# Optimization experiments

Hardware: AMD Instinct MI355X
Metric: run time of the kernel (lower is better)

The kernel has to match this reference:

```python
import jax, jax.numpy as jnp
import numpy as np

PAD = 200000   # padding index = all_features_num
D = 128        # input_dim (embedding dim)
H = 256        # hidden_dim
K = 15         # item_num (top-k)
M = 4          # multi_head


def _cos(a, b, eps=1e-8):
    # torch.cosine_similarity semantics with eps clamp on norms
    na = jnp.maximum(jnp.linalg.norm(a, axis=-1), eps)
    nb = jnp.maximum(jnp.linalg.norm(b, axis=-1), eps)
    return jnp.sum(a * b, axis=-1) / (na * nb)


def _rnn_input(x, emb):
    # x: [..., T, F] int. Fields :-2 are embedded+summed, field -2 is time.
    t = x[..., -2].astype(jnp.float32)
    dt = jnp.concatenate([jnp.zeros_like(t[..., :1]), jnp.diff(t, axis=-1)], axis=-1)
    e = emb[x[..., :-2]].sum(axis=-2)          # [..., T, D]
    x_self = e[:, 0:1, -1:, :]                  # [B,1,1,D] (self item placed at last slot of session 0)
    return jnp.concatenate([e, dt[..., None]], axis=-1), x_self


def _time_rnn(seq, W, U, b, wt, return_all=False):
    # Time-aware GRU. seq: [N, T, in+1]; last channel is delta-time feeding a decay gate.
    f, dt = seq[..., :-1], seq[..., -1:]
    N = seq.shape[0]
    g_in = jnp.einsum('nti,ij->ntj', f, W) + b   # precompute input projections [N,T,3H]

    def step(h, inp):
        g, d = inp                               # g:[N,3H], d:[N,1]
        decay = jnp.exp(-jax.nn.relu(d * wt))    # time-aware decay of hidden state
        hd = h * decay
        u = hd @ U
        z = jax.nn.sigmoid(g[:, :H] + u[:, :H])
        r = jax.nn.sigmoid(g[:, H:2 * H] + u[:, H:2 * H])
        n = jnp.tanh(g[:, 2 * H:] + r * u[:, 2 * H:])
        h_new = (1.0 - z) * hd + z * n
        return h_new, h_new

    h0 = jnp.zeros((N, H), seq.dtype)
    h_last, hs = jax.lax.scan(step, h0, (jnp.swapaxes(g_in, 0, 1), jnp.swapaxes(dt, 0, 1)))
    return jnp.swapaxes(hs, 0, 1) if return_all else h_last


def setup_inputs() -> dict:
    key = jax.random.key(0)
    ks = jax.random.split(key, 20)
    def n(k, shape, s=0.05):
        return jax.random.normal(k, shape, jnp.float32) * s
    x = jax.random.randint(ks[0], (512, 16, 64, 8), 0, PAD, dtype=jnp.int32)
    x_continuous = jax.random.randint(ks[1], (128, 128, 8), 0, PAD, dtype=jnp.int32)
    self_loc = jax.random.randint(ks[2], (512,), 0, 64, dtype=jnp.int32)
    emb = n(ks[3], (PAD + 1, D)).at[PAD].set(0.0)  # padding_idx row = 0
    return {
        'x': x, 'x_continuous': x_continuous, 'self_loc': self_loc, 'emb': emb,
        'W_rnn': n(ks[4], (2 * D, 3 * H)), 'U_rnn': n(ks[5], (H, 3 * H)), 'b_rnn': n(ks[6], (3 * H,)),
        'wt_rnn': jax.random.uniform(ks[7], (H,), jnp.float32, 0.0, 1e-5),
        'W_c': n(ks[8], (D, 3 * H)), 'U_c': n(ks[9], (H, 3 * H)), 'b_c': n(ks[10], (3 * H,)),
        'wt_c': jax.random.uniform(ks[11], (H,), jnp.float32, 0.0, 1e-5),
        'Wv': n(ks[12], (2 * H, M)), 'bv': n(ks[13], (M,)),
        'W0': n(ks[14], (D + (2 + M) * H, 1024)), 'b0': n(ks[15], (1024,)),
        'W1': n(ks[16], (1024, 512)), 'b1': n(ks[17], (512,)),
        'W2': n(ks[18], (512, 256)), 'b2': n(ks[19], (256,)),
        'Wp': n(jax.random.fold_in(key, 99), (256, 1)), 'bp': jnp.zeros((1,), jnp.float32),
    }


def reference(x, x_continuous, self_loc, emb, W_rnn, U_rnn, b_rnn, wt_rnn,
              W_c, U_c, b_c, wt_c, Wv, bv, W0, b0, W1, b1, W2, b2, Wp, bp):
    B = x.shape[0]
    label_len = B // x_continuous.shape[0]
    # ---- get_top_k: cosine sim + topk + gather ----
    real = x[..., 0] != PAD                         # [B,S,L]
    bidx = jnp.arange(B)
    e_self = emb[x[bidx, 0, self_loc, -3]]           # [B,D]
    e_items = emb[x[..., -3]]                        # [B,S,L,D]
    cos = _cos(e_self[:, None, None, :], e_items)    # [B,S,L]
    neg = jnp.min(jnp.where(real, cos, jnp.inf)) - 1.0
    sim = jnp.where(real, cos, neg)
    top_idx = jnp.sort(jax.lax.top_k(sim, K)[1], axis=-1)      # [B,S,K]
    x_top = jnp.take_along_axis(x, top_idx[..., None], axis=2)  # [B,S,K,F]
    x_top = x_top.at[:, 0, -1].set(x[bidx, 0, self_loc])
    # ---- rnn inputs ----
    xs, x_self = _rnn_input(x_top, emb)              # [B,S,K,D+1], [B,1,1,D]
    xs = jnp.concatenate([jnp.broadcast_to(x_self, xs.shape[:-1] + (D,)), xs], axis=-1)
    xs = xs.reshape(-1, K, 2 * D + 1)                # [B*S,K,2D+1]
    xc, _ = _rnn_input(x_continuous[:, None], emb)
    xc = xc[:, 0]                                    # [B',L2,D+1]
    # ---- RNNs ----
    h = _time_rnn(xs, W_rnn, U_rnn, b_rnn, wt_rnn).reshape(B, -1, H)   # [B,S,H]
    h_cont = _time_rnn(xc, W_c, U_c, b_c, wt_c, return_all=True)[:, -label_len:, :].reshape(B, H)
    # ---- multi-head attention over sessions ----
    a1 = jnp.concatenate([h, jnp.broadcast_to(h[:, :1], h.shape)], axis=-1) @ Wv + bv  # [B,S,M]
    a2 = jax.nn.softmax(jnp.tanh(a1), axis=1)
    h_att = jnp.einsum('bsm,bsh->bmh', a2, h).reshape(B, M * H)
    hh = jnp.concatenate([x_self.reshape(B, D), h[:, 0], h_att, h_cont], axis=-1)
    # ---- predict MLP (dropout = identity in eval) ----
    lr = lambda v: jnp.where(v > 0, v, 0.01 * v)     # LeakyReLU(0.01)
    z = lr(hh @ W0 + b0)
    z = lr(z @ W1 + b1)
    z = lr(z @ W2 + b2)
    return jax.nn.sigmoid(z @ Wp + bp)               # [B,1]
```

## Files before the change

kernel.cpp:

```cpp
#include <hip/hip_runtime.h>
#include <hip/hip_bf16.h>


#define PAD_TOK 200000
#define DD 128
#define HH 256
#define KK 15
#define BB 512
#define SS 16
#define II 64

typedef __bf16 bf16x8 __attribute__((ext_vector_type(8)));
typedef __bf16 bf16x4 __attribute__((ext_vector_type(4)));
typedef float f32x4 __attribute__((ext_vector_type(4)));
#define MFMA16 __builtin_amdgcn_mfma_f32_16x16x32_bf16
#define MFMA8 __builtin_amdgcn_mfma_f32_16x16x32_fp8_fp8

__device__ __forceinline__ float sigm(float x) { return 1.f / (1.f + __expf(-x)); }
__device__ __forceinline__ float tanh_fast(float x) {
  x = fminf(fmaxf(x, -15.f), 15.f);
  float e2 = __expf(2.f * x);
  return (e2 - 1.f) / (e2 + 1.f);
}
__device__ __forceinline__ float bfu(unsigned u16) { return __uint_as_float(u16 << 16); }
// ... 94 lines not shown
  if (tid < 64) {
    unsigned m = smin[tid];
    for (int o = 32; o; o >>= 1) m = min(m, __shfl_xor(m, o));
    if (tid == 0 && m != 0xFFFFFFFFu) atomicMin(minu, m);
  }
}

__global__ __launch_bounds__(64) void k_topk(const int* __restrict__ x,
                                             const float* __restrict__ simw,
                                             const unsigned* __restrict__ minu,
                                             int* __restrict__ topidx) {
  int row = blockIdx.x, i = threadIdx.x;
  unsigned mk = *minu;
  float neg = ((mk & 0x80000000u) ? __uint_as_float(mk ^ 0x80000000u) : __uint_as_float(~mk)) - 1.0f;
  float c = simw[(size_t)row * II + i];
  bool real = x[((size_t)row * II + i) * 8] != PAD_TOK;
  float s = real ? c : neg;
  __shared__ float sv[64];
  sv[i] = s;
  __syncthreads();
  int rank = 0;
  for (int j = 0; j < 64; ++j) {
    float o = sv[j];
    rank += (o > s) || (o == s && j < i);
  }
  bool sel = rank < KK;
  unsigned long long mask = __ballot(sel);
  if (sel) {
    int pos = __popcll(mask & ((1ull << i) - 1ull));
    topidx[row * KK + pos] = i;
  }
}

__global__ __launch_bounds__(128) void k_xself(const int* __restrict__ x,
                                               const int* __restrict__ self_loc,
                                               const float* __restrict__ emb,
                                               float* __restrict__ xself,
                                               __bf16* __restrict__ xself_bf) {
  int b = blockIdx.x, d = threadIdx.x;
  const int* xr = x + ((size_t)(b * SS) * II + self_loc[b]) * 8;
  float acc = 0.f;
#pragma unroll
  for (int jj = 0; jj < 6; ++jj) acc += emb[(size_t)xr[jj] * DD + d];
  xself[b * DD + d] = acc;
  xself_bf[b * DD + d] = (__bf16)acc;
}

__global__ __launch_bounds__(128) void k_build_cont(const int* __restrict__ xc,
                                                    const float* __restrict__ emb,
                                                    __hip_bfloat16* __restrict__ ec,
                                                    float* __restrict__ dtc) {
  int p = blockIdx.x, t = blockIdx.y, d = threadIdx.x;
  const int* xr = xc + ((size_t)p * 128 + t) * 8;
  float acc = 0.f;
#pragma unroll
  for (int jj = 0; jj < 6; ++jj) acc += emb[(size_t)xr[jj] * DD + d];
  ec[((size_t)p * 128 + t) * DD + d] = __float2bfloat16(acc);
  if (d == 0) dtc[p * 128 + t] = (t > 0) ? ((float)xr[6] - (float)xr[-2]) : 0.f;
}

__global__ __launch_bounds__(64) void k_pack(const float* __restrict__ B,
                                             __bf16* __restrict__ out) {
  int kt = blockIdx.x, tile = blockIdx.y, lane = threadIdx.x;
  const float* src = B + (size_t)(kt * 32 + (lane >> 4) * 8) * 768 + tile * 16 + (lane & 15);
  __bf16* o = out + (((size_t)(kt * 48 + tile) * 64 + lane) * 8);
#pragma unroll
  for (int i = 0; i < 8; ++i) o[i] = (__bf16)src[(size_t)i * 768];
}

__global__ __launch_bounds__(64) void k_pack8(const float* __restrict__ B,
                                              unsigned char* __restrict__ out) {
  int kt = blockIdx.x, tile = blockIdx.y, lane = threadIdx.x;
  const float* src = B + (size_t)(kt * 32 + (lane >> 4) * 8) * 768 + tile * 16 + (lane & 15);
  unsigned char* o = out + (((size_t)(kt * 48 + tile) * 64 + lane) * 8);
#pragma unroll
  for (int i = 0; i < 8; ++i) o[i] = f2fp8(src[(size_t)i * 768] * 8.f);
}

// ... 15 lines not shown
  const int r0 = blockIdx.x * 32;
  f32x4 z4 = {0.f, 0.f, 0.f, 0.f};
  f32x4 acc[2][6];
#pragma unroll
  for (int mt = 0; mt < 2; ++mt)
#pragma unroll
    for (int n = 0; n < 6; ++n) acc[mt][n] = z4;
#pragma unroll
  for (int kt = 0; kt < 4; ++kt) {
    bf16x8 a[2];
#pragma unroll
    for (int mt = 0; mt < 2; ++mt)
      a[mt] = *(const bf16x8*)(A + (size_t)(r0 + mt * 16 + lr) * 128 + kt * 32 + lg * 8);
#pragma unroll
    for (int n = 0; n < 6; ++n) {
      bf16x8 b = *(const bf16x8*)(pB + (((size_t)kt * 48 + wv * 6 + n) * 64 + lane) * 8);
      acc[0][n] = MFMA16(a[0], b, acc[0][n], 0, 0, 0);
      acc[1][n] = MFMA16(a[1], b, acc[1][n], 0, 0, 0);
    }
  }
#pragma unroll
  for (int mt = 0; mt < 2; ++mt)
#pragma unroll
    for (int n = 0; n < 6; ++n) {
      int col = wv * 96 + n * 16 + lr;
      int gate = col >> 8, wvc = (col >> 5) & 7, nt = (col >> 4) & 1;
      float bc = bias[col];
#pragma unroll
      for (int r = 0; r < 4; ++r) {
        int row = r0 + mt * 16 + lg * 4 + r;
        G2[(size_t)row * 1024 + wvc * 128 + lr * 8 + gate * 2 + nt] = (__bf16)(acc[mt][n][r] + bc);
      }
    }
}

__global__ __launch_bounds__(512) void k_build_gm(
    const int* __restrict__ x, const int* __restrict__ self_loc,
    const float* __restrict__ emb, const int* __restrict__ topidx,
    const __bf16* __restrict__ xself_bf, const __bf16* __restrict__ pWs,
    const __bf16* __restrict__ pWe, const float* __restrict__ bias,
    __bf16* __restrict__ Gm2, float* __restrict__ dtm) {
  const int wv = threadIdx.x >> 6, lane = threadIdx.x & 63;
  const int lr = lane & 15, lg = lane >> 4;
  const size_t rf0 = (size_t)blockIdx.x * 32;
  const int t = (int)(rf0 >> 13);
  const int n0 = (int)(rf0 & 8191);
  __shared__ __align__(16) __bf16 el[32 * 128];
  {
    int rr = threadIdx.x >> 5;
    int q = threadIdx.x & 31;
#pragma unroll
    for (int pass = 0; pass < 2; ++pass) {
      int rloc = pass * 16 + rr;
      int n = n0 + rloc;
      int b = n >> 4, s = n & 15;
      bool ovr = (s == 0) && (t == KK - 1);
      int item = ovr ? self_loc[b] : topidx[n * KK + t];
      const int* xr = x + ((size_t)n * II + item) * 8;
      float4 acc = {0.f, 0.f, 0.f, 0.f};
#pragma unroll
      for (int jj = 0; jj < 6; ++jj) {
        float4 v = *(const float4*)(emb + (size_t)xr[jj] * DD + q * 4);
        acc.x += v.x;
        acc.y += v.y;
        acc.z += v.z;
        acc.w += v.w;
      }
      bf16x4 ov = {(__bf16)acc.x, (__bf16)acc.y, (__bf16)acc.z, (__bf16)acc.w};
      *(bf16x4*)&el[(rloc * 128 + q * 4) ^ ((rloc & 7) << 3)] = ov;
      if (q == 0) {
        float dtv = 0.f;
        if (t > 0) {
          int pitem = topidx[n * KK + t - 1];
          dtv = (float)xr[6] - (float)x[((size_t)n * II + pitem) * 8 + 6];
        }
        dtm[t * 8192 + n] = dtv;
      }
    }
  }
  __syncthreads();
  f32x4 z4 = {0.f, 0.f, 0.f, 0.f};
  f32x4 acc[3][2][2];
#pragma unroll
  for (int g = 0; g < 3; ++g)
#pragma unroll
    for (int mt = 0; mt < 2; ++mt)
#pragma unroll
      for (int nt = 0; nt < 2; ++nt) acc[g][mt][nt] = z4;
#pragma unroll
  for (int kt = 0; kt < 8; ++kt) {
    bf16x8 a[2];
#pragma unroll
    for (int mt = 0; mt < 2; ++mt) {
      if (kt < 4)
        a[mt] = *(const bf16x8*)(xself_bf + (size_t)((n0 + mt * 16) >> 4) * 128 + kt * 32 + lg * 8);
      else {
        int row = mt * 16 + lr;
        a[mt] = *(const bf16x8*)&el[(row * 128 + (kt - 4) * 32 + lg * 8) ^ ((row & 7) << 3)];
      }
    }
    const __bf16* pB = (kt < 4) ? (pWs + (size_t)kt * 48 * 512) : (pWe + (size_t)(kt - 4) * 48 * 512);
#pragma unroll
    for (int g = 0; g < 3; ++g)
#pragma unroll
      for (int nt = 0; nt < 2; ++nt) {
        bf16x8 b = *(const bf16x8*)(pB + (((size_t)g * 16 + wv * 2 + nt) * 64 + lane) * 8);
#pragma unroll
        for (int mt = 0; mt < 2; ++mt) acc[g][mt][nt] = MFMA16(a[mt], b, acc[g][mt][nt], 0, 0, 0);
      }
  }
#pragma unroll
  for (int mt = 0; mt < 2; ++mt)
#pragma unroll
    for (int g = 0; g < 3; ++g)
#pragma unroll
      for (int nt = 0; nt < 2; ++nt) {
        int col = g * 256 + wv * 32 + nt * 16 + lr;
        float bc = bias[col];
#pragma unroll
        for (int r = 0; r < 4; ++r) {
          size_t rf = rf0 + mt * 16 + lg * 4 + r;
          Gm2[rf * 1024 + wv * 128 + lr * 8 + g * 2 + nt] = (__bf16)(acc[g][mt][nt][r] + bc);
        }
      }
}

__device__ void cont_body(char* smem, const __bf16* __restrict__ G2,
                          const float* __restrict__ dtc,
                          const unsigned char* __restrict__ pU8,
                          const float* __restrict__ wt, float* __restrict__ hcont,
                          int blk) {
  unsigned char(*hbuf)[16 * 256] = (unsigned char(*)[16 * 256])smem;
  unsigned char(*uL)[30 * 512] = (unsigned char(*)[30 * 512])(smem + 8192);
  float* dl = (float*)(smem + 8192 + 122880);
  const int wv = threadIdx.x >> 6, lane = threadIdx.x & 63;
  const int lr = lane & 15, lg = lane >> 4;
  const int p0 = blk * 16;
  for (int idx = threadIdx.x; idx < 2048; idx += 512)
    dl[idx] = dtc[(p0 + (idx >> 7)) * 128 + (idx & 127)];
  for (int i = threadIdx.x; i < 8 * 30 * 64; i += 512) {
    int l = i & 63;
    int fw = i >> 6;
    int f = fw % 30;
    int w = fw / 30;
    int kt = 3 + f / 6;
    int gi = f % 6;
    *(uint2*)&uL[w][(size_t)f * 512 + l * 8] =
        *(const uint2*)(pU8 + (((size_t)kt * 48 + (gi >> 1) * 16 + w * 2 + (gi & 1)) * 64 + l) * 8);
  }
  long fr[3][6];
#pragma unroll
  for (int kt = 0; kt < 3; ++kt)
#pragma unroll
    for (int gi = 0; gi < 6; ++gi)
      fr[kt][gi] =
          *(const long*)(pU8 + (((size_t)kt * 48 + (gi >> 1) * 16 + wv * 2 + (gi & 1)) * 64 + lane) * 8);

// ... 36 lines not shown
#pragma unroll
    for (int g = 0; g < 3; ++g)
#pragma unroll
      for (int nt = 0; nt < 2; ++nt) acc[g][nt] = f32x4{0.f, 0.f, 0.f, 0.f};
#pragma unroll
    for (int kt = 0; kt < 8; ++kt) {
      long a = *(const long*)&hb[lr * 256 + ((kt * 32 + lg * 8) ^ ((lr & 15) << 3))];
#pragma unroll
      for (int gi = 0; gi < 6; ++gi) {
        long b = (kt < 3) ? fr[kt][gi]
                          : *(const long*)&uL[wv][(size_t)((kt - 3) * 6 + gi) * 512 + lane * 8];
        acc[gi >> 1][gi & 1] = MFMA8(a, b, acc[gi >> 1][gi & 1], 0, 0, 0);
      }
    }
#pragma unroll
    for (int nt = 0; nt < 2; ++nt)
#pragma unroll
      for (int r = 0; r < 4; ++r) {
        unsigned uz = nt ? (Gv[r].x >> 16) : (Gv[r].x & 0xffffu);
        unsigned ur = nt ? (Gv[r].y >> 16) : (Gv[r].y & 0xffffu);
        unsigned un = nt ? (Gv[r].z >> 16) : (Gv[r].z & 0xffffu);
        const float us = 0.0078125f;
        float zz = sigm(bfu(uz) + acc[0][nt][r] * us);
        float rr = sigm(bfu(ur) + acc[1][nt][r] * us);
        float nn = tanh_fast(bfu(un) + rr * acc[2][nt][r] * us);
        float hnew = (1.f - zz) * hd[nt][r] + zz * nn;
        h[nt][r] = hnew;
        if (t >= 124)
          hcont[((size_t)(p0 + lg * 4 + r) * 4 + (t - 124)) * 256 + wv * 32 + nt * 16 + lr] = hnew;
      }
  }
}

__device__ void main_body(char* smem, const __bf16* __restrict__ Gm2,
                          const float* __restrict__ dtm, const __bf16* __restrict__ pU,
                          const float* __restrict__ wt, float* __restrict__ hmain,
                          int blk) {
  __bf16(*hbuf)[32 * 256] = (__bf16(*)[32 * 256])smem;
  float* dl = (float*)(smem + 32768);
  const int wv = threadIdx.x >> 6, lane = threadIdx.x & 63;
  const int lr = lane & 15, lg = lane >> 4;
  const int n0 = blk * 32;
  f32x4 z4 = {0.f, 0.f, 0.f, 0.f};
  for (int idx = threadIdx.x; idx < KK * 32; idx += 512)
    dl[idx] = dtm[(idx >> 5) * 8192 + n0 + (idx & 31)];
  float wtv[2];
#pragma unroll
  for (int nt = 0; nt < 2; ++nt) wtv[nt] = wt[wv * 32 + nt * 16 + lr];
  float h[2][2][4];
#pragma unroll
  for (int mt = 0; mt < 2; ++mt)
#pragma unroll
    for (int nt = 0; nt < 2; ++nt)
#pragma unroll
      for (int r = 0; r < 4; ++r) h[mt][nt][r] = 0.f;
  const uint4* Gv4 = (const uint4*)Gm2;
  __syncthreads();

  for (int t = 0; t < KK; ++t) {
    __bf16* hb = hbuf[t & 1];
#pragma unroll
    for (int mt = 0; mt < 2; ++mt)
#pragma unroll
      for (int r = 0; r < 4; ++r) {
        float dtv = dl[t * 32 + mt * 16 + lg * 4 + r];
        int row = mt * 16 + lg * 4 + r;
#pragma unroll
        for (int nt = 0; nt < 2; ++nt) {
          float hdv = h[mt][nt][r] * __expf(-fmaxf(dtv * wtv[nt], 0.f));
          hb[((row * 256) + (wv * 32 + nt * 16 + lr)) ^ ((row & 7) << 3)] = (__bf16)hdv;
        }
      }
    __syncthreads();
    f32x4 acc[3][2][2];
#pragma unroll
    for (int g = 0; g < 3; ++g)
#pragma unroll
      for (int mt = 0; mt < 2; ++mt)
#pragma unroll
        for (int nt = 0; nt < 2; ++nt) acc[g][mt][nt] = z4;
#pragma unroll
    for (int kt = 0; kt < 8; ++kt) {
      bf16x8 a[2];
#pragma unroll
      for (int mt = 0; mt < 2; ++mt) {
        int row = mt * 16 + lr;
        int s = ((row * 256) + (kt * 32 + lg * 8)) ^ ((row & 7) << 3);
        a[mt] = *(const bf16x8*)&hb[s];
      }
#pragma unroll
      for (int g = 0; g < 3; ++g)
#pragma unroll
        for (int nt = 0; nt < 2; ++nt) {
          bf16x8 b = *(const bf16x8*)(pU + (((size_t)kt * 48 + g * 16 + wv * 2 + nt) * 64 + lane) * 8);
#pragma unroll
          for (int mt = 0; mt < 2; ++mt) acc[g][mt][nt] = MFMA16(a[mt], b, acc[g][mt][nt], 0, 0, 0);
        }
    }
    uint4 Gv[2][4];
#pragma unroll
    for (int mt = 0; mt < 2; ++mt)
#pragma unroll
      for (int r = 0; r < 4; ++r)
        Gv[mt][r] = Gv4[((size_t)t * 8192 + n0 + mt * 16 + lg * 4 + r) * 128 + wv * 16 + lr];
#pragma unroll
    for (int mt = 0; mt < 2; ++mt)
#pragma unroll
      for (int r = 0; r < 4; ++r) {
        float dtv = dl[t * 32 + mt * 16 + lg * 4 + r];
#pragma unroll
        for (int nt = 0; nt < 2; ++nt) {
          unsigned uz = nt ? (Gv[mt][r].x >> 16) : (Gv[mt][r].x & 0xffffu);
          unsigned ur = nt ? (Gv[mt][r].y >> 16) : (Gv[mt][r].y & 0xffffu);
          unsigned un = nt ? (Gv[mt][r].z >> 16) : (Gv[mt][r].z & 0xffffu);
          float hdv = h[mt][nt][r] * __expf(-fmaxf(dtv * wtv[nt], 0.f));
          float zz = sigm(bfu(uz) + acc[0][mt][nt][r]);
          float rr = sigm(bfu(ur) + acc[1][mt][nt][r]);
          float nn = tanh_fast(bfu(un) + rr * acc[2][mt][nt][r]);
          h[mt][nt][r] = (1.f - zz) * hdv + zz * nn;
        }
      }
  }
  __syncthreads();
#pragma unroll
  for (int mt = 0; mt < 2; ++mt)
#pragma unroll
    for (int nt = 0; nt < 2; ++nt)
#pragma unroll
      for (int r = 0; r < 4; ++r)
        hmain[(size_t)(n0 + mt * 16 + lg * 4 + r) * 256 + wv * 32 + nt * 16 + lr] = h[mt][nt][r];
}

__global__ __launch_bounds__(512) void k_rnn_fused(
    const __bf16* __restrict__ G2, const float* __restrict__ dtc,
    const unsigned char* __restrict__ pU8, const float* __restrict__ wt_c,
    float* __restrict__ hcont, const __bf16* __restrict__ Gm2,
    const float* __restrict__ dtm, const __bf16* __restrict__ pU,
    const float* __restrict__ wt_m, float* __restrict__ hmain) {
  __shared__ __align__(16) char smem[8192 + 122880 + 8192];
  if (blockIdx.x < 8)
    cont_body(smem, G2, dtc, pU8, wt_c, hcont, blockIdx.x);
  else
    main_body(smem, Gm2, dtm, pU, wt_m, hmain, blockIdx.x - 8);
}

__global__ __launch_bounds__(256) void k_att(const float* __restrict__ hmain,
                                             const float* __restrict__ xself,
                                             const float* __restrict__ hc,
                                             const float* __restrict__ Wv,
                                             const float* __restrict__ bv,
                                             float* __restrict__ hh,
                                             __bf16* __restrict__ hh_bf) {
  int b = blockIdx.x, tid = threadIdx.x;
  __shared__ float hl[16 * 256];
  __shared__ float aa[16 * 4];
  for (int idx = tid; idx < 4096; idx += 256) hl[idx] = hmain[(size_t)b * SS * HH + idx];
  __syncthreads();
  if (tid < 64) {
    int s = tid >> 2, m = tid & 3;
    float acc = bv[m];
    for (int j = 0; j < 256; ++j)
      acc += hl[s * 256 + j] * Wv[j * 4 + m] + hl[j] * Wv[(256 + j) * 4 + m];
    aa[s * 4 + m] = tanh_fast(acc);
  }
  __syncthreads();
  if (tid < 4) {
    int m = tid;
    float mx = -1e30f;
    for (int s = 0; s < 16; ++s) mx = fmaxf(mx, aa[s * 4 + m]);
    float sum = 0.f;
    for (int s = 0; s < 16; ++s) sum += __expf(aa[s * 4 + m] - mx);
    float inv = 1.f / sum;
    for (int s = 0; s < 16; ++s) aa[s * 4 + m] = __expf(aa[s * 4 + m] - mx) * inv;
  }
  __syncthreads();
  float a0 = 0.f, a1 = 0.f, a2 = 0.f, a3 = 0.f;
// ... 89 lines not shown
  const float* U_rnn = (const float*)d_in[5];
  const float* b_rnn = (const float*)d_in[6];
  const float* wt_rnn = (const float*)d_in[7];
  const float* W_c = (const float*)d_in[8];
  const float* U_c = (const float*)d_in[9];
  const float* b_c = (const float*)d_in[10];
  const float* wt_c = (const float*)d_in[11];
  const float* Wv = (const float*)d_in[12];
  const float* bv = (const float*)d_in[13];
  const float* W0 = (const float*)d_in[14];
  const float* b0 = (const float*)d_in[15];
  const float* W1 = (const float*)d_in[16];
  const float* b1 = (const float*)d_in[17];
  const float* W2 = (const float*)d_in[18];
  const float* b2 = (const float*)d_in[19];
  const float* Wp = (const float*)d_in[20];
  const float* bp = (const float*)d_in[21];
  float* out = (float*)d_out;

  char* ws = (char*)d_ws;
  size_t cur = 0;
  auto alloc = [&](size_t bytes) {
    char* p = ws + cur;
    cur += (bytes + 255) & ~(size_t)255;
    return p;
  };
  float* es = (float*)alloc((size_t)BB * DD * 4);
  float* ns = (float*)alloc(BB * 4);
  unsigned* minu = (unsigned*)alloc(4);
  float* simw = (float*)alloc((size_t)BB * SS * II * 4);
  int* topidx = (int*)alloc((size_t)BB * SS * KK * 4);
  float* xself = (float*)alloc((size_t)BB * DD * 4);
  __bf16* xself_bf = (__bf16*)alloc((size_t)BB * DD * 2);
  float* dtm = (float*)alloc((size_t)KK * 8192 * 4);
  float* dtc = (float*)alloc((size_t)128 * 128 * 4);
  float* hcont = (float*)alloc((size_t)BB * HH * 4);
  float* hh = (float*)alloc((size_t)BB * 1664 * 4);
  __bf16* hh_bf = (__bf16*)alloc((size_t)BB * 1664 * 2);
  __bf16* z0 = (__bf16*)alloc((size_t)BB * 1024 * 2);
  __bf16* z1 = (__bf16*)alloc((size_t)BB * 512 * 2);
  __bf16* z2 = (__bf16*)alloc((size_t)BB * 256 * 2);
  float* hmain = (float*)alloc((size_t)8192 * HH * 4);
  __hip_bfloat16* ec = (__hip_bfloat16*)alloc((size_t)16384 * DD * 2);
  __bf16* G2 = (__bf16*)alloc((size_t)16384 * 1024 * 2);
  __bf16* Gm2 = (__bf16*)alloc((size_t)KK * 8192 * 1024 * 2);
  __bf16* pWs = (__bf16*)alloc((size_t)4 * 48 * 64 * 8 * 2);
  __bf16* pWe = (__bf16*)alloc((size_t)4 * 48 * 64 * 8 * 2);
  __bf16* pU = (__bf16*)alloc((size_t)8 * 48 * 64 * 8 * 2);
  __bf16* pWc = (__bf16*)alloc((size_t)4 * 48 * 64 * 8 * 2);
  unsigned char* pU8 = (unsigned char*)alloc((size_t)8 * 48 * 64 * 8);
  __bf16* pW0 = (__bf16*)alloc((size_t)52 * 64 * 64 * 8 * 2);
  __bf16* pW1 = (__bf16*)alloc((size_t)32 * 32 * 64 * 8 * 2);
  __bf16* pW2 = (__bf16*)alloc((size_t)16 * 16 * 64 * 8 * 2);
  (void)ws_size;

  hipLaunchKernelGGL(k_init, dim3(1), dim3(1), 0, stream, minu);
  hipLaunchKernelGGL(k_eself, dim3(BB), dim3(128), 0, stream, x, self_loc, emb, es, ns);
  hipLaunchKernelGGL(k_cos, dim3(BB * SS), dim3(256), 0, stream, x, emb, es, ns, simw, minu);
  hipLaunchKernelGGL(k_topk, dim3(BB * SS), dim3(64), 0, stream, x, simw, minu, topidx);
  hipLaunchKernelGGL(k_xself, dim3(BB), dim3(128), 0, stream, x, self_loc, emb, xself,
                     xself_bf);
  hipLaunchKernelGGL(k_build_cont, dim3(128, 128), dim3(128), 0, stream, xc, emb, ec, dtc);
  hipLaunchKernelGGL(k_pack, dim3(4, 48), dim3(64), 0, stream, W_rnn, pWs);
  hipLaunchKernelGGL(k_pack, dim3(4, 48), dim3(64), 0, stream, W_rnn + 128 * 768, pWe);
  hipLaunchKernelGGL(k_pack, dim3(8, 48), dim3(64), 0, stream, U_rnn, pU);
  hipLaunchKernelGGL(k_pack, dim3(4, 48), dim3(64), 0, stream, W_c, pWc);
  hipLaunchKernelGGL(k_pack8, dim3(8, 48), dim3(64), 0, stream, U_c, pU8);
  hipLaunchKernelGGL(k_packN, dim3(52, 64), dim3(64), 0, stream, W0, pW0, 1024);
  hipLaunchKernelGGL(k_packN, dim3(32, 32), dim3(64), 0, stream, W1, pW1, 512);
  hipLaunchKernelGGL(k_packN, dim3(16, 16), dim3(64), 0, stream, W2, pW2, 256);
  hipLaunchKernelGGL(k_gemm_g, dim3(512), dim3(512), 0, stream, ec, pWc, b_c, G2);
  hipLaunchKernelGGL(k_build_gm, dim3(KK * 8192 / 32), dim3(512), 0, stream, x, self_loc,
                     emb, topidx, xself_bf, pWs, pWe, b_rnn, Gm2, dtm);
  hipLaunchKernelGGL(k_rnn_fused, dim3(264), dim3(512), 0, stream, G2, dtc, pU8, wt_c,
                     hcont, Gm2, dtm, pU, wt_rnn, hmain);
  hipLaunchKernelGGL(k_att, dim3(BB), dim3(256), 0, stream, hmain, xself, hcont, Wv, bv, hh,
                     hh_bf);
  hipLaunchKernelGGL(k_mlp_mfma, dim3(4, 16), dim3(512), 0, stream, hh_bf, pW0, b0, z0,
                     1664, 1024);
  hipLaunchKernelGGL(k_mlp_mfma, dim3(2, 16), dim3(512), 0, stream, z0, pW1, b1, z1, 1024,
                     512);
  hipLaunchKernelGGL(k_mlp_mfma, dim3(1, 16), dim3(512), 0, stream, z1, pW2, b2, z2, 512,
                     256);
  hipLaunchKernelGGL(k_head, dim3(BB), dim3(64), 0, stream, z2, Wp, bp, out);
}
```

Measured before the change: 947.7 us.

## Fuse main-RNN input projection build into the fused RNN kernel

Removes the separate k_build_gm launch and instead has each main-RNN block gather embeddings, compute delta-times into shared memory, and run the input-projection MFMA for its own 32 rows across all 15 timesteps before starting the recurrence. This drops a kernel launch and the dtm global buffer, and its block-local data also removes the need for a grid-wide dependency. In exchange, the projection work that previously ran over 3840 blocks is now done by only 256 main blocks, alongside the 8 cont blocks, so parallelism for that phase is much lower. The recurrence k-loop unroll is also reduced to 2, likely to limit register pressure.

```diff
diff --git a/kernel.cpp b/kernel.cpp
--- a/kernel.cpp
+++ b/kernel.cpp
@@ -243,97 +243,6 @@
         G2[(size_t)row * 1024 + wvc * 128 + lr * 8 + gate * 2 + nt] = (__bf16)(acc[mt][n][r] + bc);
       }
     }
-}
-
-__global__ __launch_bounds__(512) void k_build_gm(
-    const int* __restrict__ x, const int* __restrict__ self_loc,
-    const float* __restrict__ emb, const int* __restrict__ topidx,
-    const __bf16* __restrict__ xself_bf, const __bf16* __restrict__ pWs,
-    const __bf16* __restrict__ pWe, const float* __restrict__ bias,
-    __bf16* __restrict__ Gm2, float* __restrict__ dtm) {
-  const int wv = threadIdx.x >> 6, lane = threadIdx.x & 63;
-  const int lr = lane & 15, lg = lane >> 4;
-  const size_t rf0 = (size_t)blockIdx.x * 32;
-  const int t = (int)(rf0 >> 13);
-  const int n0 = (int)(rf0 & 8191);
-  __shared__ __align__(16) __bf16 el[32 * 128];
-  {
-    int rr = threadIdx.x >> 5;
-    int q = threadIdx.x & 31;
-#pragma unroll
-    for (int pass = 0; pass < 2; ++pass) {
-      int rloc = pass * 16 + rr;
-      int n = n0 + rloc;
-      int b = n >> 4, s = n & 15;
-      bool ovr = (s == 0) && (t == KK - 1);
-      int item = ovr ? self_loc[b] : topidx[n * KK + t];
-      const int* xr = x + ((size_t)n * II + item) * 8;
-      float4 acc = {0.f, 0.f, 0.f, 0.f};
-#pragma unroll
-      for (int jj = 0; jj < 6; ++jj) {
-        float4 v = *(const float4*)(emb + (size_t)xr[jj] * DD + q * 4);
-        acc.x += v.x;
-        acc.y += v.y;
-        acc.z += v.z;
-        acc.w += v.w;
-      }
-      bf16x4 ov = {(__bf16)acc.x, (__bf16)acc.y, (__bf16)acc.z, (__bf16)acc.w};
-      *(bf16x4*)&el[(rloc * 128 + q * 4) ^ ((rloc & 7) << 3)] = ov;
-      if (q == 0) {
-        float dtv = 0.f;
-        if (t > 0) {
-          int pitem = topidx[n * KK + t - 1];
-          dtv = (float)xr[6] - (float)x[((size_t)n * II + pitem) * 8 + 6];
-        }
-        dtm[t * 8192 + n] = dtv;
-      }
-    }
-  }
-  __syncthreads();
-  f32x4 z4 = {0.f, 0.f, 0.f, 0.f};
-  f32x4 acc[3][2][2];
-#pragma unroll
-  for (int g = 0; g < 3; ++g)
-#pragma unroll
-    for (int mt = 0; mt < 2; ++mt)
-#pragma unroll
-      for (int nt = 0; nt < 2; ++nt) acc[g][mt][nt] = z4;
-#pragma unroll
-  for (int kt = 0; kt < 8; ++kt) {
-    bf16x8 a[2];
-#pragma unroll
-    for (int mt = 0; mt < 2; ++mt) {
-      if (kt < 4)
-        a[mt] = *(const bf16x8*)(xself_bf + (size_t)((n0 + mt * 16) >> 4) * 128 + kt * 32 + lg * 8);
-      else {
-        int row = mt * 16 + lr;
-        a[mt] = *(const bf16x8*)&el[(row * 128 + (kt - 4) * 32 + lg * 8) ^ ((row & 7) << 3)];
-      }
-    }
-    const __bf16* pB = (kt < 4) ? (pWs + (size_t)kt * 48 * 512) : (pWe + (size_t)(kt - 4) * 48 * 512);
-#pragma unroll
-    for (int g = 0; g < 3; ++g)
-#pragma unroll
-      for (int nt = 0; nt < 2; ++nt) {
-        bf16x8 b = *(const bf16x8*)(pB + (((size_t)g * 16 + wv * 2 + nt) * 64 + lane) * 8);
-#pragma unroll
-        for (int mt = 0; mt < 2; ++mt) acc[g][mt][nt] = MFMA16(a[mt], b, acc[g][mt][nt], 0, 0, 0);
-      }
-  }
-#pragma unroll
-  for (int mt = 0; mt < 2; ++mt)
-#pragma unroll
-    for (int g = 0; g < 3; ++g)
-#pragma unroll
-      for (int nt = 0; nt < 2; ++nt) {
-        int col = g * 256 + wv * 32 + nt * 16 + lr;
-        float bc = bias[col];
-#pragma unroll
-        for (int r = 0; r < 4; ++r) {
-          size_t rf = rf0 + mt * 16 + lg * 4 + r;
-          Gm2[rf * 1024 + wv * 128 + lr * 8 + g * 2 + nt] = (__bf16)(acc[g][mt][nt][r] + bc);
-        }
-      }
 }
 
 __device__ void cont_body(char* smem, const __bf16* __restrict__ G2,
@@ -436,18 +345,103 @@
   }
 }
 
-__device__ void main_body(char* smem, const __bf16* __restrict__ Gm2,
-                          const float* __restrict__ dtm, const __bf16* __restrict__ pU,
-                          const float* __restrict__ wt, float* __restrict__ hmain,
-                          int blk) {
+__device__ void main_body(char* smem, const int* __restrict__ x,
+                          const int* __restrict__ self_loc,
+                          const float* __restrict__ emb,
+                          const int* __restrict__ topidx,
+                          const __bf16* __restrict__ xself_bf,
+                          const __bf16* __restrict__ pWs, const __bf16* __restrict__ pWe,
+                          const float* __restrict__ gbias, __bf16* __restrict__ Gm2,
+                          const __bf16* __restrict__ pU, const float* __restrict__ wt,
+                          float* __restrict__ hmain, int blk) {
   __bf16(*hbuf)[32 * 256] = (__bf16(*)[32 * 256])smem;
+  __bf16* el = (__bf16*)smem;
   float* dl = (float*)(smem + 32768);
   const int wv = threadIdx.x >> 6, lane = threadIdx.x & 63;
   const int lr = lane & 15, lg = lane >> 4;
   const int n0 = blk * 32;
   f32x4 z4 = {0.f, 0.f, 0.f, 0.f};
-  for (int idx = threadIdx.x; idx < KK * 32; idx += 512)
-    dl[idx] = dtm[(idx >> 5) * 8192 + n0 + (idx & 31)];
+  const uint4* Gv4 = (const uint4*)Gm2;
+
+  for (int t = 0; t < KK; ++t) {
+    {
+      int rr = threadIdx.x >> 5, q = threadIdx.x & 31;
+#pragma unroll
+      for (int pass = 0; pass < 2; ++pass) {
+        int rloc = pass * 16 + rr;
+        int n = n0 + rloc;
+        int b = n >> 4, s = n & 15;
+        bool ovr = (s == 0) && (t == KK - 1);
+        int item = ovr ? self_loc[b] : topidx[n * KK + t];
+        const int* xr = x + ((size_t)n * II + item) * 8;
+        float4 a4 = {0.f, 0.f, 0.f, 0.f};
+#pragma unroll
+        for (int jj = 0; jj < 6; ++jj) {
+          float4 v = *(const float4*)(emb + (size_t)xr[jj] * DD + q * 4);
+          a4.x += v.x;
+          a4.y += v.y;
+          a4.z += v.z;
+          a4.w += v.w;
+        }
+        bf16x4 ov = {(__bf16)a4.x, (__bf16)a4.y, (__bf16)a4.z, (__bf16)a4.w};
+        *(bf16x4*)&el[(rloc * 128 + q * 4) ^ ((rloc & 7) << 3)] = ov;
+        if (q == 0) {
+          float dtv = 0.f;
+          if (t > 0) {
+            int pitem = topidx[n * KK + t - 1];
+            dtv = (float)xr[6] - (float)x[((size_t)n * II + pitem) * 8 + 6];
+          }
+          dl[t * 32 + rloc] = dtv;
+        }
+      }
+    }
+    __syncthreads();
+    f32x4 acc[3][2][2];
+#pragma unroll
+    for (int g = 0; g < 3; ++g)
+#pragma unroll
+      for (int mt = 0; mt < 2; ++mt)
+#pragma unroll
+        for (int nt = 0; nt < 2; ++nt) acc[g][mt][nt] = z4;
+#pragma unroll
+    for (int kt = 0; kt < 8; ++kt) {
+      bf16x8 a[2];
+#pragma unroll
+      for (int mt = 0; mt < 2; ++mt) {
+        if (kt < 4)
+          a[mt] = *(const bf16x8*)(xself_bf + (size_t)((n0 + mt * 16) >> 4) * 128 + kt * 32 + lg * 8);
+        else {
+          int row = mt * 16 + lr;
+          a[mt] = *(const bf16x8*)&el[(row * 128 + (kt - 4) * 32 + lg * 8) ^ ((row & 7) << 3)];
+        }
+      }
+      const __bf16* pB = (kt < 4) ? (pWs + (size_t)kt * 48 * 512) : (pWe + (size_t)(kt - 4) * 48 * 512);
+#pragma unroll
+      for (int g = 0; g < 3; ++g)
+#pragma unroll
+        for (int nt = 0; nt < 2; ++nt) {
+          bf16x8 b = *(const bf16x8*)(pB + (((size_t)g * 16 + wv * 2 + nt) * 64 + lane) * 8);
+#pragma unroll
+          for (int mt = 0; mt < 2; ++mt) acc[g][mt][nt] = MFMA16(a[mt], b, acc[g][mt][nt], 0, 0, 0);
+        }
+    }
+#pragma unroll
+    for (int mt = 0; mt < 2; ++mt)
+#pragma unroll
+      for (int g = 0; g < 3; ++g)
+#pragma unroll
+        for (int nt = 0; nt < 2; ++nt) {
+          int col = g * 256 + wv * 32 + nt * 16 + lr;
+          float bc = gbias[col];
+#pragma unroll
+          for (int r = 0; r < 4; ++r) {
+            size_t rf = (size_t)t * 8192 + n0 + mt * 16 + lg * 4 + r;
+            Gm2[rf * 1024 + wv * 128 + lr * 8 + g * 2 + nt] = (__bf16)(acc[g][mt][nt][r] + bc);
+          }
+        }
+    __syncthreads();
+  }
+
   float wtv[2];
 #pragma unroll
   for (int nt = 0; nt < 2; ++nt) wtv[nt] = wt[wv * 32 + nt * 16 + lr];
@@ -458,8 +452,6 @@
     for (int nt = 0; nt < 2; ++nt)
 #pragma unroll
       for (int r = 0; r < 4; ++r) h[mt][nt][r] = 0.f;
-  const uint4* Gv4 = (const uint4*)Gm2;
-  __syncthreads();
 
   for (int t = 0; t < KK; ++t) {
     __bf16* hb = hbuf[t & 1];
@@ -483,7 +475,7 @@
       for (int mt = 0; mt < 2; ++mt)
 #pragma unroll
         for (int nt = 0; nt < 2; ++nt) acc[g][mt][nt] = z4;
-#pragma unroll
+#pragma unroll 2
     for (int kt = 0; kt < 8; ++kt) {
       bf16x8 a[2];
 #pragma unroll
@@ -538,14 +530,19 @@
 __global__ __launch_bounds__(512) void k_rnn_fused(
     const __bf16* __restrict__ G2, const float* __restrict__ dtc,
     const unsigned char* __restrict__ pU8, const float* __restrict__ wt_c,
-    float* __restrict__ hcont, const __bf16* __restrict__ Gm2,
-    const float* __restrict__ dtm, const __bf16* __restrict__ pU,
-    const float* __restrict__ wt_m, float* __restrict__ hmain) {
+    float* __restrict__ hcont, const int* __restrict__ x,
+    const int* __restrict__ self_loc, const float* __restrict__ emb,
+    const int* __restrict__ topidx, const __bf16* __restrict__ xself_bf,
+    const __bf16* __restrict__ pWs, const __bf16* __restrict__ pWe,
+    const float* __restrict__ b_rnn, __bf16* __restrict__ Gm2,
+    const __bf16* __restrict__ pU, const float* __restrict__ wt_m,
+    float* __restrict__ hmain) {
   __shared__ __align__(16) char smem[8192 + 122880 + 8192];
   if (blockIdx.x < 8)
     cont_body(smem, G2, dtc, pU8, wt_c, hcont, blockIdx.x);
   else
-    main_body(smem, Gm2, dtm, pU, wt_m, hmain, blockIdx.x - 8);
+    main_body(smem, x, self_loc, emb, topidx, xself_bf, pWs, pWe, b_rnn, Gm2, pU, wt_m,
+              hmain, blockIdx.x - 8);
 }
 
 __global__ __launch_bounds__(256) void k_att(const float* __restrict__ hmain,
@@ -701,7 +698,6 @@
   int* topidx = (int*)alloc((size_t)BB * SS * KK * 4);
   float* xself = (float*)alloc((size_t)BB * DD * 4);
   __bf16* xself_bf = (__bf16*)alloc((size_t)BB * DD * 2);
-  float* dtm = (float*)alloc((size_t)KK * 8192 * 4);
   float* dtc = (float*)alloc((size_t)128 * 128 * 4);
   float* hcont = (float*)alloc((size_t)BB * HH * 4);
   float* hh = (float*)alloc((size_t)BB * 1664 * 4);
@@ -739,10 +735,9 @@
   hipLaunchKernelGGL(k_packN, dim3(32, 32), dim3(64), 0, stream, W1, pW1, 512);
   hipLaunchKernelGGL(k_packN, dim3(16, 16), dim3(64), 0, stream, W2, pW2, 256);
   hipLaunchKernelGGL(k_gemm_g, dim3(512), dim3(512), 0, stream, ec, pWc, b_c, G2);
-  hipLaunchKernelGGL(k_build_gm, dim3(KK * 8192 / 32), dim3(512), 0, stream, x, self_loc,
-                     emb, topidx, xself_bf, pWs, pWe, b_rnn, Gm2, dtm);
   hipLaunchKernelGGL(k_rnn_fused, dim3(264), dim3(512), 0, stream, G2, dtc, pU8, wt_c,
-                     hcont, Gm2, dtm, pU, wt_rnn, hmain);
+                     hcont, x, self_loc, emb, topidx, xself_bf, pWs, pWe, b_rnn, Gm2, pU,
+                     wt_rnn, hmain);
   hipLaunchKernelGGL(k_att, dim3(BB), dim3(256), 0, stream, hmain, xself, hcont, Wv, bv, hh,
                      hh_bf);
   hipLaunchKernelGGL(k_mlp_mfma, dim3(4, 16), dim3(512), 0, stream, hh_bf, pW0, b0, z0,
```

New measurement: 0.9997 ms. 1.05x slower.

## Fuse main GRU input projection into recurrent kernel, drop Gm2 buffer

Applied to the files above, without the earlier changes.

Removes the separate input-projection GEMM kernel that wrote a large bf16 gate tensor (15×8192×1024), and instead computes the input projection (xself and item embedding against W) inside the recurrent loop, reading compact bf16 embeddings. A new gather kernel builds the embeddings, dt, and xself, replacing k_xself. This trades a large HBM write and read for extra MFMA work on the sequential recurrent path. The GEMM is also split over two n-tile passes to keep register pressure down, and the n-gate recurrent product is kept apart from its input product.

```diff
diff --git a/kernel.cpp b/kernel.cpp
--- a/kernel.cpp
+++ b/kernel.cpp
@@ -150,18 +150,47 @@
   }
 }
 
-__global__ __launch_bounds__(128) void k_xself(const int* __restrict__ x,
-                                               const int* __restrict__ self_loc,
-                                               const float* __restrict__ emb,
-                                               float* __restrict__ xself,
-                                               __bf16* __restrict__ xself_bf) {
-  int b = blockIdx.x, d = threadIdx.x;
-  const int* xr = x + ((size_t)(b * SS) * II + self_loc[b]) * 8;
-  float acc = 0.f;
-#pragma unroll
-  for (int jj = 0; jj < 6; ++jj) acc += emb[(size_t)xr[jj] * DD + d];
-  xself[b * DD + d] = acc;
-  xself_bf[b * DD + d] = (__bf16)acc;
+__global__ __launch_bounds__(256) void k_build_main(const int* __restrict__ x,
+                                                    const int* __restrict__ self_loc,
+                                                    const float* __restrict__ emb,
+                                                    const int* __restrict__ topidx,
+                                                    __bf16* __restrict__ em,
+                                                    float* __restrict__ dtm,
+                                                    float* __restrict__ xself,
+                                                    __bf16* __restrict__ xself_bf) {
+  int t = blockIdx.y;
+  int n = blockIdx.x * 8 + (threadIdx.x >> 5);
+  int q = threadIdx.x & 31;
+  int b = n >> 4, s = n & 15;
+  bool ovr = (s == 0) && (t == KK - 1);
+  int item = ovr ? self_loc[b] : topidx[n * KK + t];
+  const int* xr = x + ((size_t)n * II + item) * 8;
+  int toks[6];
+#pragma unroll
+  for (int jj = 0; jj < 6; ++jj) toks[jj] = xr[jj];
+  float4 acc = {0.f, 0.f, 0.f, 0.f};
+#pragma unroll
+  for (int jj = 0; jj < 6; ++jj) {
+    float4 v = *(const float4*)(emb + (size_t)toks[jj] * DD + q * 4);
+    acc.x += v.x;
+    acc.y += v.y;
+    acc.z += v.z;
+    acc.w += v.w;
+  }
+  bf16x4 ov = {(__bf16)acc.x, (__bf16)acc.y, (__bf16)acc.z, (__bf16)acc.w};
+  *(bf16x4*)(em + ((size_t)t * 8192 + n) * DD + q * 4) = ov;
+  if (ovr) {
+    *(float4*)(xself + b * DD + q * 4) = acc;
+    *(bf16x4*)(xself_bf + b * DD + q * 4) = ov;
+  }
+  if (q == 0) {
+    float dtv = 0.f;
+    if (t > 0) {
+      int pitem = topidx[n * KK + t - 1];
+      dtv = (float)xr[6] - (float)x[((size_t)n * II + pitem) * 8 + 6];
+    }
+    dtm[t * 8192 + n] = dtv;
+  }
 }
 
 __global__ __launch_bounds__(128) void k_build_cont(const int* __restrict__ xc,
@@ -243,97 +272,6 @@
         G2[(size_t)row * 1024 + wvc * 128 + lr * 8 + gate * 2 + nt] = (__bf16)(acc[mt][n][r] + bc);
       }
     }
-}
-
-__global__ __launch_bounds__(512) void k_build_gm(
-    const int* __restrict__ x, const int* __restrict__ self_loc,
-    const float* __restrict__ emb, const int* __restrict__ topidx,
-    const __bf16* __restrict__ xself_bf, const __bf16* __restrict__ pWs,
-    const __bf16* __restrict__ pWe, const float* __restrict__ bias,
-    __bf16* __restrict__ Gm2, float* __restrict__ dtm) {
-  const int wv = threadIdx.x >> 6, lane = threadIdx.x & 63;
-  const int lr = lane & 15, lg = lane >> 4;
-  const size_t rf0 = (size_t)blockIdx.x * 32;
-  const int t = (int)(rf0 >> 13);
-  const int n0 = (int)(rf0 & 8191);
-  __shared__ __align__(16) __bf16 el[32 * 128];
-  {
-    int rr = threadIdx.x >> 5;
-    int q = threadIdx.x & 31;
-#pragma unroll
-    for (int pass = 0; pass < 2; ++pass) {
-      int rloc = pass * 16 + rr;
-      int n = n0 + rloc;
-      int b = n >> 4, s = n & 15;
-      bool ovr = (s == 0) && (t == KK - 1);
-      int item = ovr ? self_loc[b] : topidx[n * KK + t];
-      const int* xr = x + ((size_t)n * II + item) * 8;
-      float4 acc = {0.f, 0.f, 0.f, 0.f};
-#pragma unroll
-      for (int jj = 0; jj < 6; ++jj) {
-        float4 v = *(const float4*)(emb + (size_t)xr[jj] * DD + q * 4);
-        acc.x += v.x;
-        acc.y += v.y;
-        acc.z += v.z;
-        acc.w += v.w;
-      }
-      bf16x4 ov = {(__bf16)acc.x, (__bf16)acc.y, (__bf16)acc.z, (__bf16)acc.w};
-      *(bf16x4*)&el[(rloc * 128 + q * 4) ^ ((rloc & 7) << 3)] = ov;
-      if (q == 0) {
-        float dtv = 0.f;
-        if (t > 0) {
-          int pitem = topidx[n * KK + t - 1];
-          dtv = (float)xr[6] - (float)x[((size_t)n * II + pitem) * 8 + 6];
-        }
-        dtm[t * 8192 + n] = dtv;
-      }
-    }
-  }
-  __syncthreads();
-  f32x4 z4 = {0.f, 0.f, 0.f, 0.f};
-  f32x4 acc[3][2][2];
-#pragma unroll
-  for (int g = 0; g < 3; ++g)
-#pragma unroll
-    for (int mt = 0; mt < 2; ++mt)
-#pragma unroll
-      for (int nt = 0; nt < 2; ++nt) acc[g][mt][nt] = z4;
-#pragma unroll
-  for (int kt = 0; kt < 8; ++kt) {
-    bf16x8 a[2];
-#pragma unroll
-    for (int mt = 0; mt < 2; ++mt) {
-      if (kt < 4)
-        a[mt] = *(const bf16x8*)(xself_bf + (size_t)((n0 + mt * 16) >> 4) * 128 + kt * 32 + lg * 8);
-      else {
-        int row = mt * 16 + lr;
-        a[mt] = *(const bf16x8*)&el[(row * 128 + (kt - 4) * 32 + lg * 8) ^ ((row & 7) << 3)];
-      }
-    }
-    const __bf16* pB = (kt < 4) ? (pWs + (size_t)kt * 48 * 512) : (pWe + (size_t)(kt - 4) * 48 * 512);
-#pragma unroll
-    for (int g = 0; g < 3; ++g)
-#pragma unroll
-      for (int nt = 0; nt < 2; ++nt) {
-        bf16x8 b = *(const bf16x8*)(pB + (((size_t)g * 16 + wv * 2 + nt) * 64 + lane) * 8);
-#pragma unroll
-        for (int mt = 0; mt < 2; ++mt) acc[g][mt][nt] = MFMA16(a[mt], b, acc[g][mt][nt], 0, 0, 0);
-      }
-  }
-#pragma unroll
-  for (int mt = 0; mt < 2; ++mt)
-#pragma unroll
-    for (int g = 0; g < 3; ++g)
-#pragma unroll
-      for (int nt = 0; nt < 2; ++nt) {
-        int col = g * 256 + wv * 32 + nt * 16 + lr;
-        float bc = bias[col];
-#pragma unroll
-        for (int r = 0; r < 4; ++r) {
-          size_t rf = rf0 + mt * 16 + lg * 4 + r;
-          Gm2[rf * 1024 + wv * 128 + lr * 8 + g * 2 + nt] = (__bf16)(acc[g][mt][nt][r] + bc);
-        }
-      }
 }
 
 __device__ void cont_body(char* smem, const __bf16* __restrict__ G2,
@@ -436,8 +374,11 @@
   }
 }
 
-__device__ void main_body(char* smem, const __bf16* __restrict__ Gm2,
-                          const float* __restrict__ dtm, const __bf16* __restrict__ pU,
+__device__ void main_body(char* smem, const __bf16* __restrict__ em,
+                          const float* __restrict__ dtm,
+                          const __bf16* __restrict__ xself_bf,
+                          const __bf16* __restrict__ pWs, const __bf16* __restrict__ pWe,
+                          const __bf16* __restrict__ pU, const float* __restrict__ bg,
                           const float* __restrict__ wt, float* __restrict__ hmain,
                           int blk) {
   __bf16(*hbuf)[32 * 256] = (__bf16(*)[32 * 256])smem;
@@ -448,9 +389,15 @@
   f32x4 z4 = {0.f, 0.f, 0.f, 0.f};
   for (int idx = threadIdx.x; idx < KK * 32; idx += 512)
     dl[idx] = dtm[(idx >> 5) * 8192 + n0 + (idx & 31)];
-  float wtv[2];
-#pragma unroll
-  for (int nt = 0; nt < 2; ++nt) wtv[nt] = wt[wv * 32 + nt * 16 + lr];
+  float wtv[2], bz[2], br[2], bn[2];
+#pragma unroll
+  for (int nt = 0; nt < 2; ++nt) {
+    int c = wv * 32 + nt * 16 + lr;
+    wtv[nt] = wt[c];
+    bz[nt] = bg[c];
+    br[nt] = bg[c + 256];
+    bn[nt] = bg[c + 512];
+  }
   float h[2][2][4];
 #pragma unroll
   for (int mt = 0; mt < 2; ++mt)
@@ -458,7 +405,6 @@
     for (int nt = 0; nt < 2; ++nt)
 #pragma unroll
       for (int r = 0; r < 4; ++r) h[mt][nt][r] = 0.f;
-  const uint4* Gv4 = (const uint4*)Gm2;
   __syncthreads();
 
   for (int t = 0; t < KK; ++t) {
@@ -476,54 +422,63 @@
         }
       }
     __syncthreads();
-    f32x4 acc[3][2][2];
-#pragma unroll
-    for (int g = 0; g < 3; ++g)
-#pragma unroll
-      for (int mt = 0; mt < 2; ++mt)
-#pragma unroll
-        for (int nt = 0; nt < 2; ++nt) acc[g][mt][nt] = z4;
-#pragma unroll
-    for (int kt = 0; kt < 8; ++kt) {
-      bf16x8 a[2];
-#pragma unroll
-      for (int mt = 0; mt < 2; ++mt) {
-        int row = mt * 16 + lr;
-        int s = ((row * 256) + (kt * 32 + lg * 8)) ^ ((row & 7) << 3);
-        a[mt] = *(const bf16x8*)&hb[s];
-      }
-#pragma unroll
-      for (int g = 0; g < 3; ++g)
-#pragma unroll
-        for (int nt = 0; nt < 2; ++nt) {
-          bf16x8 b = *(const bf16x8*)(pU + (((size_t)kt * 48 + g * 16 + wv * 2 + nt) * 64 + lane) * 8);
-#pragma unroll
-          for (int mt = 0; mt < 2; ++mt) acc[g][mt][nt] = MFMA16(a[mt], b, acc[g][mt][nt], 0, 0, 0);
+
+#pragma unroll
+    for (int ntp = 0; ntp < 2; ++ntp) {
+      f32x4 acc[4][2];
+#pragma unroll
+      for (int a4 = 0; a4 < 4; ++a4)
+#pragma unroll
+        for (int mt = 0; mt < 2; ++mt) acc[a4][mt] = z4;
+#pragma unroll 2
+      for (int kt = 0; kt < 8; ++kt) {
+        bf16x8 a[2];
+#pragma unroll
+        for (int mt = 0; mt < 2; ++mt) {
+          int row = mt * 16 + lr;
+          int s = ((row * 256) + (kt * 32 + lg * 8)) ^ ((row & 7) << 3);
+          a[mt] = *(const bf16x8*)&hb[s];
         }
-    }
-    uint4 Gv[2][4];
-#pragma unroll
-    for (int mt = 0; mt < 2; ++mt)
-#pragma unroll
-      for (int r = 0; r < 4; ++r)
-        Gv[mt][r] = Gv4[((size_t)t * 8192 + n0 + mt * 16 + lg * 4 + r) * 128 + wv * 16 + lr];
-#pragma unroll
-    for (int mt = 0; mt < 2; ++mt)
-#pragma unroll
-      for (int r = 0; r < 4; ++r) {
-        float dtv = dl[t * 32 + mt * 16 + lg * 4 + r];
-#pragma unroll
-        for (int nt = 0; nt < 2; ++nt) {
-          unsigned uz = nt ? (Gv[mt][r].x >> 16) : (Gv[mt][r].x & 0xffffu);
-          unsigned ur = nt ? (Gv[mt][r].y >> 16) : (Gv[mt][r].y & 0xffffu);
-          unsigned un = nt ? (Gv[mt][r].z >> 16) : (Gv[mt][r].z & 0xffffu);
-          float hdv = h[mt][nt][r] * __expf(-fmaxf(dtv * wtv[nt], 0.f));
-          float zz = sigm(bfu(uz) + acc[0][mt][nt][r]);
-          float rr = sigm(bfu(ur) + acc[1][mt][nt][r]);
-          float nn = tanh_fast(bfu(un) + rr * acc[2][mt][nt][r]);
-          h[mt][nt][r] = (1.f - zz) * hdv + zz * nn;
+#pragma unroll
+        for (int g = 0; g < 3; ++g) {
+          const int ai = (g < 2) ? g : 3;
+          bf16x8 b = *(const bf16x8*)(pU + (((size_t)kt * 48 + g * 16 + wv * 2 + ntp) * 64 + lane) * 8);
+#pragma unroll
+          for (int mt = 0; mt < 2; ++mt) acc[ai][mt] = MFMA16(a[mt], b, acc[ai][mt], 0, 0, 0);
         }
       }
+#pragma unroll 2
+      for (int kt = 0; kt < 8; ++kt) {
+        bf16x8 a[2];
+#pragma unroll
+        for (int mt = 0; mt < 2; ++mt) {
+          if (kt < 4)
+            a[mt] = *(const bf16x8*)(xself_bf + (size_t)((n0 + mt * 16) >> 4) * 128 + kt * 32 + lg * 8);
+          else
+            a[mt] = *(const bf16x8*)(em + ((size_t)t * 8192 + n0 + mt * 16 + lr) * 128 +
+                                     (kt - 4) * 32 + lg * 8);
+        }
+        const __bf16* pB = (kt < 4) ? (pWs + (size_t)kt * 48 * 512)
+                                    : (pWe + (size_t)(kt - 4) * 48 * 512);
+#pragma unroll
+        for (int g = 0; g < 3; ++g) {
+          bf16x8 b = *(const bf16x8*)(pB + (((size_t)g * 16 + wv * 2 + ntp) * 64 + lane) * 8);
+#pragma unroll
+          for (int mt = 0; mt < 2; ++mt) acc[g][mt] = MFMA16(a[mt], b, acc[g][mt], 0, 0, 0);
+        }
+      }
+#pragma unroll
+      for (int mt = 0; mt < 2; ++mt)
+#pragma unroll
+        for (int r = 0; r < 4; ++r) {
+          float dtv = dl[t * 32 + mt * 16 + lg * 4 + r];
+          float hdv = h[mt][ntp][r] * __expf(-fmaxf(dtv * wtv[ntp], 0.f));
+          float zz = sigm(acc[0][mt][r] + bz[ntp]);
+          float rr = sigm(acc[1][mt][r] + br[ntp]);
+          float nn = tanh_fast(acc[2][mt][r] + bn[ntp] + rr * acc[3][mt][r]);
+          h[mt][ntp][r] = (1.f - zz) * hdv + zz * nn;
+        }
+    }
   }
   __syncthreads();
 #pragma unroll
@@ -538,14 +493,16 @@
 __global__ __launch_bounds__(512) void k_rnn_fused(
     const __bf16* __restrict__ G2, const float* __restrict__ dtc,
     const unsigned char* __restrict__ pU8, const float* __restrict__ wt_c,
-    float* __restrict__ hcont, const __bf16* __restrict__ Gm2,
-    const float* __restrict__ dtm, const __bf16* __restrict__ pU,
+    float* __restrict__ hcont, const __bf16* __restrict__ em,
+    const float* __restrict__ dtm, const __bf16* __restrict__ xself_bf,
+    const __bf16* __restrict__ pWs, const __bf16* __restrict__ pWe,
+    const __bf16* __restrict__ pU, const float* __restrict__ b_rnn,
     const float* __restrict__ wt_m, float* __restrict__ hmain) {
   __shared__ __align__(16) char smem[8192 + 122880 + 8192];
   if (blockIdx.x < 8)
     cont_body(smem, G2, dtc, pU8, wt_c, hcont, blockIdx.x);
   else
-    main_body(smem, Gm2, dtm, pU, wt_m, hmain, blockIdx.x - 8);
+    main_body(smem, em, dtm, xself_bf, pWs, pWe, pU, b_rnn, wt_m, hmain, blockIdx.x - 8);
 }
 
 __global__ __launch_bounds__(256) void k_att(const float* __restrict__ hmain,
@@ -711,8 +668,8 @@
   __bf16* z2 = (__bf16*)alloc((size_t)BB * 256 * 2);
   float* hmain = (float*)alloc((size_t)8192 * HH * 4);
   __hip_bfloat16* ec = (__hip_bfloat16*)alloc((size_t)16384 * DD * 2);
+  __bf16* em = (__bf16*)alloc((size_t)KK * 8192 * DD * 2);
   __bf16* G2 = (__bf16*)alloc((size_t)16384 * 1024 * 2);
-  __bf16* Gm2 = (__bf16*)alloc((size_t)KK * 8192 * 1024 * 2);
   __bf16* pWs = (__bf16*)alloc((size_t)4 * 48 * 64 * 8 * 2);
   __bf16* pWe = (__bf16*)alloc((size_t)4 * 48 * 64 * 8 * 2);
   __bf16* pU = (__bf16*)alloc((size_t)8 * 48 * 64 * 8 * 2);
@@ -727,8 +684,8 @@
   hipLaunchKernelGGL(k_eself, dim3(BB), dim3(128), 0, stream, x, self_loc, emb, es, ns);
   hipLaunchKernelGGL(k_cos, dim3(BB * SS), dim3(256), 0, stream, x, emb, es, ns, simw, minu);
   hipLaunchKernelGGL(k_topk, dim3(BB * SS), dim3(64), 0, stream, x, simw, minu, topidx);
-  hipLaunchKernelGGL(k_xself, dim3(BB), dim3(128), 0, stream, x, self_loc, emb, xself,
-                     xself_bf);
+  hipLaunchKernelGGL(k_build_main, dim3(1024, KK), dim3(256), 0, stream, x, self_loc, emb,
+                     topidx, em, dtm, xself, xself_bf);
   hipLaunchKernelGGL(k_build_cont, dim3(128, 128), dim3(128), 0, stream, xc, emb, ec, dtc);
   hipLaunchKernelGGL(k_pack, dim3(4, 48), dim3(64), 0, stream, W_rnn, pWs);
   hipLaunchKernelGGL(k_pack, dim3(4, 48), dim3(64), 0, stream, W_rnn + 128 * 768, pWe);
@@ -739,10 +696,8 @@
   hipLaunchKernelGGL(k_packN, dim3(32, 32), dim3(64), 0, stream, W1, pW1, 512);
   hipLaunchKernelGGL(k_packN, dim3(16, 16), dim3(64), 0, stream, W2, pW2, 256);
   hipLaunchKernelGGL(k_gemm_g, dim3(512), dim3(512), 0, stream, ec, pWc, b_c, G2);
-  hipLaunchKernelGGL(k_build_gm, dim3(KK * 8192 / 32), dim3(512), 0, stream, x, self_loc,
-                     emb, topidx, xself_bf, pWs, pWe, b_rnn, Gm2, dtm);
   hipLaunchKernelGGL(k_rnn_fused, dim3(264), dim3(512), 0, stream, G2, dtc, pU8, wt_c,
-                     hcont, Gm2, dtm, pU, wt_rnn, hmain);
+                     hcont, em, dtm, xself_bf, pWs, pWe, pU, b_rnn, wt_rnn, hmain);
   hipLaunchKernelGGL(k_att, dim3(BB), dim3(256), 0, stream, hmain, xself, hcont, Wv, bv, hh,
                      hh_bf);
   hipLaunchKernelGGL(k_mlp_mfma, dim3(4, 16), dim3(512), 0, stream, hh_bf, pW0, b0, z0,
```

Measured after the change: 774.4 us. -18.3%, faster.
